# Performance work log

Measured on AMD Instinct MI355X. Metric: run time of the kernel, lower is better.

Reference implementation:

```python
import jax, jax.numpy as jnp
import numpy as np

D_G, D_2D, D_3D = 512, 768, 1024
D_F, RANK, ATTN_H = 256, 16, 512
B = 8192


def _xavier(key, shape):
    fan_out, fan_in = shape
    lim = float(np.sqrt(6.0 / (fan_in + fan_out)))
    return jax.random.uniform(key, shape, jnp.float32, -lim, lim)


def setup_inputs() -> dict:
    key = jax.random.key(0)
    ks = jax.random.split(key, 12)
    inp = {
        "h_g": jax.random.normal(ks[0], (B, D_G), jnp.float32),
        "h_2d": jax.random.normal(ks[1], (B, D_2D), jnp.float32),
        "h_3d": jax.random.normal(ks[2], (B, D_3D), jnp.float32),
        # modality projections (torch Linear: y = x @ W.T + b)
        "Wg": _xavier(ks[3], (D_F, D_G)),   "bg": jnp.zeros((D_F,), jnp.float32),
        "W2": _xavier(ks[4], (D_F, D_2D)),  "b2": jnp.zeros((D_F,), jnp.float32),
        "W3": _xavier(ks[5], (D_F, D_3D)),  "b3": jnp.zeros((D_F,), jnp.float32),
        # LayerNorm affine params
        "ln_g_w": jnp.ones((D_F,), jnp.float32),  "ln_g_b": jnp.zeros((D_F,), jnp.float32),
        "ln_2_w": jnp.ones((D_F,), jnp.float32),  "ln_2_b": jnp.zeros((D_F,), jnp.float32),
        "ln_3_w": jnp.ones((D_F,), jnp.float32),  "ln_3_b": jnp.zeros((D_F,), jnp.float32),
        # rank expansions (no bias)
        "U": _xavier(ks[6], (RANK * D_F, D_F)),
        "V": _xavier(ks[7], (RANK * D_F, D_F)),
        "S": _xavier(ks[8], (RANK * D_F, D_F)),
        # attention MLP
        "Wa1": _xavier(ks[9], (ATTN_H, D_G + D_2D + D_3D)), "ba1": jnp.zeros((ATTN_H,), jnp.float32),
        "Wa2": _xavier(ks[10], (RANK, ATTN_H)),             "ba2": jnp.zeros((RANK,), jnp.float32),
    }
    return inp


def _layernorm(x, w, b, eps=1e-5):
    mu = jnp.mean(x, axis=-1, keepdims=True)
    var = jnp.var(x, axis=-1, keepdims=True)
    return (x - mu) * jax.lax.rsqrt(var + eps) * w + b


def reference(h_g, h_2d, h_3d, Wg, bg, W2, b2, W3, b3,
              ln_g_w, ln_g_b, ln_2_w, ln_2_b, ln_3_w, ln_3_b,
              U, V, S, Wa1, ba1, Wa2, ba2):
    # proj + LN + ReLU (dropout=0 / eval mode)
    g = jax.nn.relu(_layernorm(h_g @ Wg.T + bg, ln_g_w, ln_g_b))
    d2 = jax.nn.relu(_layernorm(h_2d @ W2.T + b2, ln_2_w, ln_2_b))
    d3 = jax.nn.relu(_layernorm(h_3d @ W3.T + b3, ln_3_w, ln_3_b))
    b = g.shape[0]
    # rank expansion: (B, R, d_f)
    g_r = (g @ U.T).reshape(b, RANK, D_F)
    d2_r = (d2 @ V.T).reshape(b, RANK, D_F)
    d3_r = (d3 @ S.T).reshape(b, RANK, D_F)
    z_r = g_r * d2_r * d3_r  # elementwise tri-linear product
    # rank attention from raw modality concat
    h_cat = jnp.concatenate([h_g, h_2d, h_3d], axis=-1)
    beta = jax.nn.softmax(jax.nn.relu(h_cat @ Wa1.T + ba1) @ Wa2.T + ba2, axis=-1)  # (B, R)
    z = jnp.einsum('brd,br->bd', z_r, beta)  # (B, d_f)
    return z
```

## Files before the change

### kernel.cpp

```cpp
#include <hip/hip_runtime.h>
#include <stdint.h>

#define B_ROWS 8192
#define DG 512
#define D2 768
#define D3 1024
#define DCAT 2304
#define DF 256
#define RANK 16
#define AH 512

#define OFF_WG 0
#define OFF_W2 131072
#define OFF_W3 327680
#define OFF_U  589824
#define OFF_V  1638400
#define OFF_S  2686976
#define OFF_WA1 3735552

#define WS_WBUF  0u
#define WS_GBUF  9830400u
#define WS_A1P   22413312u
#define WS_ZPART 22413312u
#define WS_BETA  55967744u
#define WS_REQUIRED 94240768u

typedef __attribute__((ext_vector_type(8))) short short8;
typedef __attribute__((ext_vector_type(4))) float f32x4;

__device__ inline unsigned short f2bf(float f) {
  union { float f; unsigned int u; } v; v.f = f;
  unsigned int u = v.u + 0x7fffu + ((v.u >> 16) & 1u);
  return (unsigned short)(u >> 16);
}
__device__ inline float bf2f(unsigned short h) {
  union { float f; unsigned int u; } v; v.u = ((unsigned int)h) << 16;
  return v.f;
}

typedef const unsigned int __attribute__((address_space(1)))* as1_u32p;
typedef unsigned int __attribute__((address_space(3)))* as3_u32p;

__device__ inline void g2l16(const unsigned short* g, unsigned short* l) {
  __builtin_amdgcn_global_load_lds((as1_u32p)g, (as3_u32p)l, 16, 0, 0);
}


__global__ __launch_bounds__(256) void cvt_w_k(const float* __restrict__ Wg,
                                               const float* __restrict__ W2,
                                               const float* __restrict__ W3,
                                               const float* __restrict__ U,
                                               const float* __restrict__ V,
                                               const float* __restrict__ S,
                                               const float* __restrict__ Wa1,
                                               unsigned short* __restrict__ wbuf) {
  const int e = (blockIdx.x * 256 + threadIdx.x) * 4;
  const float* src;
  if (e < OFF_W2)       src = Wg  + e;
  else if (e < OFF_W3)  src = W2  + (e - OFF_W2);
  else if (e < OFF_U)   src = W3  + (e - OFF_W3);
  else if (e < OFF_V)   src = U   + (e - OFF_U);
  else if (e < OFF_S)   src = V   + (e - OFF_V);
  else if (e < OFF_WA1) src = S   + (e - OFF_S);
  else                  src = Wa1 + (e - OFF_WA1);
  float4 v = *(const float4*)src;
  ushort4 o;
  o.x = f2bf(v.x); o.y = f2bf(v.y); o.z = f2bf(v.z); o.w = f2bf(v.w);
  *(ushort4*)(wbuf + e) = o;
}


__global__ __launch_bounds__(512, 2) void fatgemm256_k(const float* __restrict__ hgf,
                                                       const float* __restrict__ h2f,
                                                       const float* __restrict__ h3f,
                                                       const unsigned short* __restrict__ wbuf,
                                                       const float* __restrict__ bg,
                                                       const float* __restrict__ b2,
                                                       const float* __restrict__ b3,
                                                       const float* __restrict__ wg,
                                                       const float* __restrict__ wbg,
                                                       const float* __restrict__ w2,
                                                       const float* __restrict__ wb2,
                                                       const float* __restrict__ w3,
                                                       const float* __restrict__ wb3,
                                                       unsigned short* __restrict__ gout,
                                                       unsigned short* __restrict__ a1part) {
  __shared__ __align__(16) unsigned short lA[2 * 256 * 64];
  __shared__ __align__(16) unsigned short lB[2 * 256 * 64];
  const int bid = blockIdx.x;
  const int tid = threadIdx.x;
  const int lane = tid & 63;
  const int wid = tid >> 6;
  const int wr = wid >> 2;
  const int wc = wid & 3;
  const int row_s = tid >> 3;
  const int kc_s = (((tid & 7) ^ (row_s & 7)) << 3);
  const int mbase = wr * 128 + (lane & 15);
  const int nbase = wc * 64 + (lane & 15);
  const int kq = lane >> 4;
  const int h = lane & 7;

  int role_a1 = 0, half = 0, m0 = 0, n0 = 0, z = 0, nt = 0;
  if (bid < 64)       { role_a1 = 1; half = 0; n0 = (bid & 1) << 8; m0 = (bid >> 1) << 8; nt = 20; }
  else if (bid < 96)  { z = 2; m0 = (bid - 64) << 8; nt = 16; }
  else if (bid < 160) { role_a1 = 1; half = 1; int r6 = bid - 96; n0 = (r6 & 1) << 8; m0 = (r6 >> 1) << 8; nt = 16; }
  else if (bid < 192) { z = 1; m0 = (bid - 160) << 8; nt = 12; }
  else                { z = 0; m0 = (bid - 192) << 8; nt = 8; }

  const float* projA = (z == 0) ? hgf : ((z == 1) ? h2f : h3f);
  const int Kz   = (z == 0) ? DG : ((z == 1) ? D2 : D3);
  const int woff = (z == 0) ? OFF_WG : ((z == 1) ? OFF_W2 : OFF_W3);

  float4 ar[8];
  auto loadA = [&](int t) {
    const float* Ag; int lda; int ka;
    if (role_a1) {
      const int tt = half ? (20 + t) : t;
      if (tt < 8)       { Ag = hgf; lda = DG; ka = tt * 64; }
      else if (tt < 20) { Ag = h2f; lda = D2; ka = (tt - 8) * 64; }
      else              { Ag = h3f; lda = D3; ka = (tt - 20) * 64; }
      Ag += (size_t)m0 * lda;
    } else {
      lda = Kz; Ag = projA + (size_t)m0 * lda; ka = t * 64;
    }
#pragma unroll
    for (int q = 0; q < 4; ++q) {
      const float* src = Ag + (size_t)(q * 64 + row_s) * lda + ka + kc_s;
      ar[q * 2]     = *(const float4*)src;
      ar[q * 2 + 1] = *(const float4*)(src + 4);
    }
  };

  auto writeA = [&](unsigned short* dA) {
#pragma unroll
    for (int q = 0; q < 4; ++q) {
      const float4 a = ar[q * 2], b = ar[q * 2 + 1];
      short8 w;
      w[0] = (short)f2bf(a.x); w[1] = (short)f2bf(a.y);
      w[2] = (short)f2bf(a.z); w[3] = (short)f2bf(a.w);
      w[4] = (short)f2bf(b.x); w[5] = (short)f2bf(b.y);
      w[6] = (short)f2bf(b.z); w[7] = (short)f2bf(b.w);
      *(short8*)(dA + (q * 512 + tid) * 8) = w;
    }
  };

  auto stageB = [&](int t, unsigned short* dB) {
    const unsigned short* Bg; int ldb; int kb;
    if (role_a1) {
      const int tt = half ? (20 + t) : t;
      Bg = wbuf + OFF_WA1 + (size_t)n0 * DCAT; ldb = DCAT; kb = tt * 64;
    } else {
      Bg = wbuf + woff; ldb = Kz; kb = t * 64;
    }
#pragma unroll
    for (int q = 0; q < 4; ++q)
      g2l16(Bg + (size_t)(q * 64 + row_s) * ldb + kb + kc_s, dB + (q * 512 + tid) * 8);
  };

  f32x4 acc[8][4];
#pragma unroll
  for (int ti = 0; ti < 8; ++ti)
#pragma unroll
    for (int tj = 0; tj < 4; ++tj)
      acc[ti][tj] = (f32x4){0.f, 0.f, 0.f, 0.f};

  auto compute = [&](const unsigned short* sA, const unsigned short* sB) {
#pragma unroll
    for (int kk = 0; kk < 2; ++kk) {
      const int kch = (kk << 2) + kq;
      const int ko = ((kch ^ h) << 3);
      short8 af[8], bfr[4];
#pragma unroll
      for (int t4 = 0; t4 < 8; ++t4)
        af[t4] = *(const short8*)(sA + (mbase + t4 * 16) * 64 + ko);
#pragma unroll
      for (int t4 = 0; t4 < 4; ++t4)
        bfr[t4] = *(const short8*)(sB + (nbase + t4 * 16) * 64 + ko);
      __builtin_amdgcn_s_setprio(1);
#pragma unroll
      for (int ti = 0; ti < 8; ++ti)
#pragma unroll
        for (int tj = 0; tj < 4; ++tj)
          acc[ti][tj] = __builtin_amdgcn_mfma_f32_16x16x32_bf16(af[ti], bfr[tj], acc[ti][tj], 0, 0, 0);
      __builtin_amdgcn_s_setprio(0);
    }
  };

  stageB(0, lB);
  loadA(0);
  stageB(1, lB + 16384);

  for (int t = 0; t < nt; ++t) {
    const int b = t & 1;
    unsigned short* cA = lA + b * 16384;
    unsigned short* cB = lB + b * 16384;
    if (t + 1 < nt) asm volatile("s_waitcnt vmcnt(4)" ::: "memory");
    else            asm volatile("s_waitcnt vmcnt(0)" ::: "memory");
    __builtin_amdgcn_sched_barrier(0);
    writeA(cA);
    if (t + 1 < nt) loadA(t + 1);
    asm volatile("s_waitcnt lgkmcnt(0)" ::: "memory");
    __builtin_amdgcn_s_barrier();
    __builtin_amdgcn_sched_barrier(0);
    compute(cA, cB);
    __builtin_amdgcn_sched_barrier(0);
    __builtin_amdgcn_s_barrier();
    if (t + 2 < nt) stageB(t + 2, cB);
  }

  if (role_a1) {
    unsigned short* out = a1part + (size_t)half * (B_ROWS * AH);
    const int r0 = m0 + wr * 128 + ((lane >> 4) << 2);
    const int c0 = n0 + wc * 64 + (lane & 15);
#pragma unroll
    for (int ti = 0; ti < 8; ++ti)
#pragma unroll
      for (int tj = 0; tj < 4; ++tj)
#pragma unroll
        for (int i = 0; i < 4; ++i)
          out[(size_t)(r0 + ti * 16 + i) * AH + (c0 + tj * 16)] = f2bf(acc[ti][tj][i]);
  } else {
    const float* bias = (z == 0) ? bg : ((z == 1) ? b2 : b3);
    const float* lnw  = (z == 0) ? wg : ((z == 1) ? w2 : w3);
    const float* lnb  = (z == 0) ? wbg : ((z == 1) ? wb2 : wb3);
    const int cbase = wc * 64 + (lane & 15);
    float bs[4], lw4[4], lb4[4];
#pragma unroll
    for (int tj = 0; tj < 4; ++tj) {
      const int col = cbase + tj * 16;
      bs[tj] = bias[col]; lw4[tj] = lnw[col]; lb4[tj] = lnb[col];
    }
#pragma unroll
    for (int ti = 0; ti < 8; ++ti)
#pragma unroll
      for (int tj = 0; tj < 4; ++tj)
#pragma unroll
        for (int i = 0; i < 4; ++i)
          acc[ti][tj][i] += bs[tj];

    float* lnr = (float*)lA;
    __syncthreads();
#pragma unroll
    for (int ti = 0; ti < 8; ++ti)
#pragma unroll
      for (int i = 0; i < 4; ++i) {
        float s = acc[ti][0][i] + acc[ti][1][i] + acc[ti][2][i] + acc[ti][3][i];
        float q = acc[ti][0][i] * acc[ti][0][i] + acc[ti][1][i] * acc[ti][1][i]
                + acc[ti][2][i] * acc[ti][2][i] + acc[ti][3][i] * acc[ti][3][i];
#pragma unroll
        for (int m = 1; m < 16; m <<= 1) { s += __shfl_xor(s, m, 64); q += __shfl_xor(q, m, 64); }
        if ((lane & 15) == 0) {
          const int rl = wr * 128 + ti * 16 + ((lane >> 4) << 2) + i;
          lnr[rl * 8 + wc * 2]     = s;
          lnr[rl * 8 + wc * 2 + 1] = q;
        }
      }
    __syncthreads();
    unsigned short* gz = gout + (size_t)z * (B_ROWS * DF);
#pragma unroll
    for (int ti = 0; ti < 8; ++ti)
#pragma unroll
      for (int i = 0; i < 4; ++i) {
        const int rl = wr * 128 + ti * 16 + ((lane >> 4) << 2) + i;
        const float4 pa = *(const float4*)(lnr + rl * 8);
        const float4 pb = *(const float4*)(lnr + rl * 8 + 4);
        const float sum = pa.x + pa.z + pb.x + pb.z;
        const float sq  = pa.y + pa.w + pb.y + pb.w;
        const float mean = sum * (1.f / DF);
        const float var  = sq * (1.f / DF) - mean * mean;
        const float rs   = rsqrtf(var + 1e-5f);
        const size_t rowoff = (size_t)(m0 + rl) * DF;
#pragma unroll
        for (int tj = 0; tj < 4; ++tj) {
          const float v = (acc[ti][tj][i] - mean) * rs * lw4[tj] + lb4[tj];
          gz[rowoff + cbase + tj * 16] = f2bf(fmaxf(v, 0.f));
        }
      }
  }
}


__global__ __launch_bounds__(256, 2) void rank_fused_k(const unsigned short* __restrict__ gbuf,
                                                       const unsigned short* __restrict__ wbuf,
                                                       const float* __restrict__ beta,
                                                       float* __restrict__ zpart) {
  __shared__ __align__(16) unsigned short lA[2 * 128 * 64];
  __shared__ __align__(16) unsigned short lB[2 * 128 * 64];
  __shared__ float lbeta[4 * 128];
  const int m0 = blockIdx.x * 128;
  const int d0 = blockIdx.y * 128;
  const int rg = blockIdx.z * 4;
  const int tid = threadIdx.x;

  for (int i = tid; i < 512; i += 256) {
    const int rr = i >> 7, row = i & 127;
    lbeta[i] = beta[(size_t)(m0 + row) * RANK + rg + rr];
  }
  __syncthreads();

  const int lane = tid & 63;
  const int wr = tid >> 7, wc = (tid >> 6) & 1;
  const int row_s = tid >> 3;
  const int kc_s = (((tid & 7) ^ ((tid >> 3) & 7)) << 3);
  const int mbase = wr * 64 + (lane & 15);
  const int nbase = wc * 64 + (lane & 15);
  const int kq = lane >> 4;
  const int h = lane & 7;
  const int lr0 = wr * 64 + ((lane >> 4) << 2);

  const unsigned short* Abase = gbuf + (size_t)(m0 + row_s) * DF + kc_s;
  const unsigned short* Bbase = wbuf + OFF_U + (size_t)(rg * 256 + d0 + row_s) * DF + kc_s;

  auto stage = [&](int t, unsigned short* dA, unsigned short* dB) {
    const int p = t >> 2, ks = t & 3;
    const int rr = p / 3;
    const int zi = p - rr * 3;
    const unsigned short* Ag = Abase + (size_t)zi * (B_ROWS * DF) + ks * 64;
    const unsigned short* Bg = Bbase + (size_t)zi * 1048576 + (size_t)rr * (256 * DF) + ks * 64;
#pragma unroll
    for (int q = 0; q < 4; ++q) {
      const int lofs = (q * 256 + tid) * 8;
      g2l16(Ag + (size_t)q * 32 * DF, dA + lofs);
      g2l16(Bg + (size_t)q * 32 * DF, dB + lofs);
    }
  };

  f32x4 zacc[4][4], prod[4][4], acc[4][4];
#pragma unroll
  for (int ti = 0; ti < 4; ++ti)
#pragma unroll
    for (int tj = 0; tj < 4; ++tj) {
      zacc[ti][tj] = (f32x4){0.f, 0.f, 0.f, 0.f};
      acc[ti][tj]  = (f32x4){0.f, 0.f, 0.f, 0.f};
    }

  auto compute = [&](const unsigned short* sA, const unsigned short* sB) {
#pragma unroll
    for (int kk = 0; kk < 2; ++kk) {
      const int kch = (kk << 2) + kq;
      const int ko = ((kch ^ h) << 3);
      short8 af[4], bfr[4];
#pragma unroll
      for (int t4 = 0; t4 < 4; ++t4) {
        af[t4]  = *(const short8*)(sA + (mbase + t4 * 16) * 64 + ko);
        bfr[t4] = *(const short8*)(sB + (nbase + t4 * 16) * 64 + ko);
      }
      __builtin_amdgcn_s_setprio(1);
#pragma unroll
      for (int ti = 0; ti < 4; ++ti)
#pragma unroll
        for (int tj = 0; tj < 4; ++tj)
          acc[ti][tj] = __builtin_amdgcn_mfma_f32_16x16x32_bf16(af[ti], bfr[tj], acc[ti][tj], 0, 0, 0);
      __builtin_amdgcn_s_setprio(0);
    }
  };

  stage(0, lA, lB);
  stage(1, lA + 8192, lB + 8192);

  for (int p = 0; p < 12; ++p) {
    const int rr = p / 3;
    const int zi = p - rr * 3;
#pragma unroll
    for (int ks = 0; ks < 4; ++ks) {
      const int t = (p << 2) + ks;
      const int b = t & 1;
      unsigned short* cA = lA + b * 8192;
      unsigned short* cB = lB + b * 8192;
      if (t < 47) asm volatile("s_waitcnt vmcnt(8)" ::: "memory");
      else        asm volatile("s_waitcnt vmcnt(0)" ::: "memory");
      __builtin_amdgcn_s_barrier();
      __builtin_amdgcn_sched_barrier(0);
      compute(cA, cB);
      __builtin_amdgcn_sched_barrier(0);
      __builtin_amdgcn_s_barrier();
      if (t + 2 < 48) stage(t + 2, cA, cB);
    }

    if (zi == 0) {
#pragma unroll
      for (int ti = 0; ti < 4; ++ti)
#pragma unroll
        for (int tj = 0; tj < 4; ++tj)
          prod[ti][tj] = acc[ti][tj];
    } else if (zi == 1) {
#pragma unroll
      for (int ti = 0; ti < 4; ++ti)
#pragma unroll
        for (int tj = 0; tj < 4; ++tj)
          prod[ti][tj] *= acc[ti][tj];
    } else {
#pragma unroll
      for (int ti = 0; ti < 4; ++ti) {
        const float4 b4 = *(const float4*)(lbeta + rr * 128 + lr0 + ti * 16);
        const float bv[4] = {b4.x, b4.y, b4.z, b4.w};
#pragma unroll
        for (int tj = 0; tj < 4; ++tj)
#pragma unroll
          for (int i = 0; i < 4; ++i)
            zacc[ti][tj][i] += prod[ti][tj][i] * acc[ti][tj][i] * bv[i];
      }
    }
#pragma unroll
    for (int ti = 0; ti < 4; ++ti)
#pragma unroll
      for (int tj = 0; tj < 4; ++tj)
        acc[ti][tj] = (f32x4){0.f, 0.f, 0.f, 0.f};
  }

  float* zp = zpart + (size_t)blockIdx.z * (B_ROWS * DF);
  const int c0 = d0 + wc * 64 + (lane & 15);
#pragma unroll
  for (int ti = 0; ti < 4; ++ti)
#pragma unroll
    for (int tj = 0; tj < 4; ++tj)
#pragma unroll
      for (int i = 0; i < 4; ++i)
        zp[(size_t)(m0 + lr0 + ti * 16 + i) * DF + (c0 + tj * 16)] = zacc[ti][tj][i];
}


__global__ __launch_bounds__(256) void zsum_k(const float* __restrict__ zpart,
                                              float* __restrict__ z) {
  const int idx = blockIdx.x * 256 + threadIdx.x;
  const size_t e = (size_t)idx * 4;
  const size_t stride = (size_t)B_ROWS * DF;
  float4 a = *(const float4*)(zpart + e);
  float4 b = *(const float4*)(zpart + stride + e);
  float4 c = *(const float4*)(zpart + 2 * stride + e);
  float4 d = *(const float4*)(zpart + 3 * stride + e);
  float4 o;
  o.x = (a.x + b.x) + (c.x + d.x);
  o.y = (a.y + b.y) + (c.y + d.y);
  o.z = (a.z + b.z) + (c.z + d.z);
  o.w = (a.w + b.w) + (c.w + d.w);
  *(float4*)(z + e) = o;
}


__global__ __launch_bounds__(256) void post_beta_k(const unsigned short* __restrict__ a1part,
                                                   const float* __restrict__ ba1,
                                                   const float* __restrict__ Wa2,
                                                   const float* __restrict__ ba2,
                                                   float* __restrict__ beta) {
  __shared__ float lw[RANK * AH];
  for (int i = threadIdx.x; i < RANK * AH / 4; i += 256)
    *(float4*)(lw + i * 4) = *(const float4*)(Wa2 + i * 4);
  __syncthreads();
  const int row = blockIdx.x * 4 + (threadIdx.x >> 6);
  const int lane = threadIdx.x & 63;
  const unsigned short* h0 = a1part + (size_t)row * AH + lane * 8;
  const unsigned short* h1 = h0 + (size_t)B_ROWS * AH;
  const uint4 p0 = *(const uint4*)h0;
  const uint4 p1 = *(const uint4*)h1;
  const unsigned int u0[4] = {p0.x, p0.y, p0.z, p0.w};
  const unsigned int u1[4] = {p1.x, p1.y, p1.z, p1.w};
  float4 ca = *(const float4*)(ba1 + lane * 8);
  float4 cb = *(const float4*)(ba1 + lane * 8 + 4);
  const float bias[8] = {ca.x, ca.y, ca.z, ca.w, cb.x, cb.y, cb.z, cb.w};
  float av[8];
#pragma unroll
  for (int j = 0; j < 4; ++j) {
    const float s0 = bf2f((unsigned short)(u0[j] & 0xffffu)) + bf2f((unsigned short)(u1[j] & 0xffffu));
    const float s1 = bf2f((unsigned short)(u0[j] >> 16)) + bf2f((unsigned short)(u1[j] >> 16));
    av[2 * j]     = fmaxf(s0 + bias[2 * j], 0.f);
    av[2 * j + 1] = fmaxf(s1 + bias[2 * j + 1], 0.f);
  }
  float lg[RANK];
#pragma unroll
  for (int r = 0; r < RANK; ++r) {
    const float* wrow = lw + r * AH + lane * 8;
    float4 wa = *(const float4*)wrow;
    float4 wb = *(const float4*)(wrow + 4);
    float p = av[0] * wa.x + av[1] * wa.y + av[2] * wa.z + av[3] * wa.w
            + av[4] * wb.x + av[5] * wb.y + av[6] * wb.z + av[7] * wb.w;
#pragma unroll
    for (int m = 1; m < 64; m <<= 1) p += __shfl_xor(p, m, 64);
    lg[r] = p + ba2[r];
  }
  float mx = lg[0];
#pragma unroll
  for (int r = 1; r < RANK; ++r) mx = fmaxf(mx, lg[r]);
  float den = 0.f;
#pragma unroll
  for (int r = 0; r < RANK; ++r) { lg[r] = __expf(lg[r] - mx); den += lg[r]; }
  const float inv = 1.f / den;
  if (lane < RANK) {
    float mine = 0.f;
#pragma unroll
    for (int r = 0; r < RANK; ++r) mine = (lane == r) ? lg[r] : mine;
    beta[(size_t)row * RANK + lane] = mine * inv;
  }
}


extern "C" void kernel_launch(void* const* d_in, const int* in_sizes, int n_in,
                              void* d_out, int out_size, void* d_ws, size_t ws_size,
                              hipStream_t stream) {
  if (ws_size < (size_t)WS_REQUIRED) return;

  const float* h_g   = (const float*)d_in[0];
  const float* h_2d  = (const float*)d_in[1];
  const float* h_3d  = (const float*)d_in[2];
  const float* Wg    = (const float*)d_in[3];
  const float* bg    = (const float*)d_in[4];
  const float* W2    = (const float*)d_in[5];
  const float* b2    = (const float*)d_in[6];
  const float* W3    = (const float*)d_in[7];
  const float* b3    = (const float*)d_in[8];
  const float* ln_g_w = (const float*)d_in[9];
  const float* ln_g_b = (const float*)d_in[10];
  const float* ln_2_w = (const float*)d_in[11];
  const float* ln_2_b = (const float*)d_in[12];
  const float* ln_3_w = (const float*)d_in[13];
  const float* ln_3_b = (const float*)d_in[14];
  const float* U     = (const float*)d_in[15];
  const float* V     = (const float*)d_in[16];
  const float* S     = (const float*)d_in[17];
  const float* Wa1   = (const float*)d_in[18];
  const float* ba1   = (const float*)d_in[19];
  const float* Wa2   = (const float*)d_in[20];
  const float* ba2   = (const float*)d_in[21];

  char* ws = (char*)d_ws;
  unsigned short* wbuf   = (unsigned short*)(ws + WS_WBUF);
  unsigned short* gbuf   = (unsigned short*)(ws + WS_GBUF);
  unsigned short* a1part = (unsigned short*)(ws + WS_A1P);
  float*          zpart  = (float*)(ws + WS_ZPART);
  float*          beta   = (float*)(ws + WS_BETA);
  float* z = (float*)d_out;

  cvt_w_k<<<dim3(4800), dim3(256), 0, stream>>>(Wg, W2, W3, U, V, S, Wa1, wbuf);
  fatgemm256_k<<<dim3(224), dim3(512), 0, stream>>>(h_g, h_2d, h_3d, wbuf,
                                                    bg, b2, b3,
                                                    ln_g_w, ln_g_b, ln_2_w, ln_2_b,
                                                    ln_3_w, ln_3_b,
                                                    gbuf, a1part);
  post_beta_k<<<dim3(2048), dim3(256), 0, stream>>>(a1part, ba1, Wa2, ba2, beta);
  rank_fused_k<<<dim3(64, 2, 4), dim3(256), 0, stream>>>(gbuf, wbuf, beta, zpart);
  zsum_k<<<dim3(2048), dim3(256), 0, stream>>>(zpart, z);
}
```

Measured before the change: 287.3 us.

## Fuse partial-sum reduction into rank kernel via atomic tickets; rebalance attention K-split

Removes the separate zsum kernel launch. The last of the four rank-group blocks for each output tile, chosen by an atomic ticket counter, sums the four partials and writes z. The attention-hidden GEMM blocks now split K evenly (18 tiles per half) instead of 20/16, which balances block work inside the fat GEMM. Workspace offsets move so zpart no longer aliases a1part, and a memset is added to clear the tickets. The cost is extra fences and atomics, plus a tail where only one block per tile does the reduction.

```diff
diff --git a/kernel.cpp b/kernel.cpp
--- a/kernel.cpp
+++ b/kernel.cpp
@@ -21,8 +21,9 @@
 #define WS_WBUF  0u
 #define WS_GBUF  9830400u
 #define WS_A1P   22413312u
-#define WS_ZPART 22413312u
-#define WS_BETA  55967744u
+#define WS_ZPART 39190528u
+#define WS_BETA  72744960u
+#define WS_TICK  73269248u
 #define WS_REQUIRED 94240768u
 
 typedef __attribute__((ext_vector_type(8))) short short8;
@@ -101,9 +102,9 @@
   const int h = lane & 7;
 
   int role_a1 = 0, half = 0, m0 = 0, n0 = 0, z = 0, nt = 0;
-  if (bid < 64)       { role_a1 = 1; half = 0; n0 = (bid & 1) << 8; m0 = (bid >> 1) << 8; nt = 20; }
-  else if (bid < 96)  { z = 2; m0 = (bid - 64) << 8; nt = 16; }
-  else if (bid < 160) { role_a1 = 1; half = 1; int r6 = bid - 96; n0 = (r6 & 1) << 8; m0 = (r6 >> 1) << 8; nt = 16; }
+  if (bid < 128)      { role_a1 = 1; half = bid >> 6; int r6 = bid & 63;
+                        n0 = (r6 & 1) << 8; m0 = (r6 >> 1) << 8; nt = 18; }
+  else if (bid < 160) { z = 2; m0 = (bid - 128) << 8; nt = 16; }
   else if (bid < 192) { z = 1; m0 = (bid - 160) << 8; nt = 12; }
   else                { z = 0; m0 = (bid - 192) << 8; nt = 8; }
 
@@ -115,7 +116,7 @@
   auto loadA = [&](int t) {
     const float* Ag; int lda; int ka;
     if (role_a1) {
-      const int tt = half ? (20 + t) : t;
+      const int tt = half * 18 + t;
       if (tt < 8)       { Ag = hgf; lda = DG; ka = tt * 64; }
       else if (tt < 20) { Ag = h2f; lda = D2; ka = (tt - 8) * 64; }
       else              { Ag = h3f; lda = D3; ka = (tt - 20) * 64; }
@@ -147,7 +148,7 @@
   auto stageB = [&](int t, unsigned short* dB) {
     const unsigned short* Bg; int ldb; int kb;
     if (role_a1) {
-      const int tt = half ? (20 + t) : t;
+      const int tt = half * 18 + t;
       Bg = wbuf + OFF_WA1 + (size_t)n0 * DCAT; ldb = DCAT; kb = tt * 64;
     } else {
       Bg = wbuf + woff; ldb = Kz; kb = t * 64;
@@ -283,10 +284,13 @@
 __global__ __launch_bounds__(256, 2) void rank_fused_k(const unsigned short* __restrict__ gbuf,
                                                        const unsigned short* __restrict__ wbuf,
                                                        const float* __restrict__ beta,
-                                                       float* __restrict__ zpart) {
+                                                       float* __restrict__ zpart,
+                                                       float* __restrict__ z,
+                                                       unsigned int* __restrict__ tickets) {
   __shared__ __align__(16) unsigned short lA[2 * 128 * 64];
   __shared__ __align__(16) unsigned short lB[2 * 128 * 64];
   __shared__ float lbeta[4 * 128];
+  __shared__ unsigned int ticket;
   const int m0 = blockIdx.x * 128;
   const int d0 = blockIdx.y * 128;
   const int rg = blockIdx.z * 4;
@@ -417,24 +421,27 @@
 #pragma unroll
       for (int i = 0; i < 4; ++i)
         zp[(size_t)(m0 + lr0 + ti * 16 + i) * DF + (c0 + tj * 16)] = zacc[ti][tj][i];
-}
-
-
-__global__ __launch_bounds__(256) void zsum_k(const float* __restrict__ zpart,
-                                              float* __restrict__ z) {
-  const int idx = blockIdx.x * 256 + threadIdx.x;
-  const size_t e = (size_t)idx * 4;
-  const size_t stride = (size_t)B_ROWS * DF;
-  float4 a = *(const float4*)(zpart + e);
-  float4 b = *(const float4*)(zpart + stride + e);
-  float4 c = *(const float4*)(zpart + 2 * stride + e);
-  float4 d = *(const float4*)(zpart + 3 * stride + e);
-  float4 o;
-  o.x = (a.x + b.x) + (c.x + d.x);
-  o.y = (a.y + b.y) + (c.y + d.y);
-  o.z = (a.z + b.z) + (c.z + d.z);
-  o.w = (a.w + b.w) + (c.w + d.w);
-  *(float4*)(z + e) = o;
+
+  __threadfence();
+  if (tid == 0) ticket = atomicAdd(&tickets[blockIdx.x * 2 + blockIdx.y], 1u);
+  __syncthreads();
+  if (ticket == 3u) {
+    __threadfence();
+    const size_t stride = (size_t)B_ROWS * DF;
+#pragma unroll
+    for (int ti = 0; ti < 4; ++ti)
+#pragma unroll
+      for (int tj = 0; tj < 4; ++tj)
+#pragma unroll
+        for (int i = 0; i < 4; ++i) {
+          const size_t off = (size_t)(m0 + lr0 + ti * 16 + i) * DF + (c0 + tj * 16);
+          const float p0 = zpart[off];
+          const float p1 = zpart[stride + off];
+          const float p2 = zpart[2 * stride + off];
+          const float p3 = zpart[3 * stride + off];
+          z[off] = (p0 + p1) + (p2 + p3);
+        }
+  }
 }
 
 
@@ -528,7 +535,10 @@
   unsigned short* a1part = (unsigned short*)(ws + WS_A1P);
   float*          zpart  = (float*)(ws + WS_ZPART);
   float*          beta   = (float*)(ws + WS_BETA);
+  unsigned int*   tick   = (unsigned int*)(ws + WS_TICK);
   float* z = (float*)d_out;
+
+  hipMemsetAsync(tick, 0, 512, stream);
 
   cvt_w_k<<<dim3(4800), dim3(256), 0, stream>>>(Wg, W2, W3, U, V, S, Wa1, wbuf);
   fatgemm256_k<<<dim3(224), dim3(512), 0, stream>>>(h_g, h_2d, h_3d, wbuf,
@@ -537,6 +547,5 @@
                                                     ln_3_w, ln_3_b,
                                                     gbuf, a1part);
   post_beta_k<<<dim3(2048), dim3(256), 0, stream>>>(a1part, ba1, Wa2, ba2, beta);
-  rank_fused_k<<<dim3(64, 2, 4), dim3(256), 0, stream>>>(gbuf, wbuf, beta, zpart);
-  zsum_k<<<dim3(2048), dim3(256), 0, stream>>>(zpart, z);
-}
+  rank_fused_k<<<dim3(64, 2, 4), dim3(256), 0, stream>>>(gbuf, wbuf, beta, zpart, z, tick);
+}
```

Result: slower. 371.5 us (+29.3%).
